# Optimization experiments

Measured on AMD Instinct MI355X. Metric: run time of the kernel, lower is better.

The kernel has to match this reference:

```python
import jax, jax.numpy as jnp
import numpy as np


def setup_inputs() -> dict:
    key = jax.random.key(0)
    k1, k2 = jax.random.split(key)
    x = jax.random.normal(k1, (16, 64, 224, 224), dtype=jnp.float32)
    # conv weight [out=1, in=2, kh=7, kw=7]; init roughly mimics small-normal init
    conv_w = jax.random.normal(k2, (1, 2, 7, 7), dtype=jnp.float32) * 0.01
    conv_b = jnp.zeros((1,), dtype=jnp.float32)
    return {"x": x, "conv_w": conv_w, "conv_b": conv_b}


def reference(x, conv_w, conv_b):
    # channel-wise mean and max -> [B, 2, H, W]
    avg_out = jnp.mean(x, axis=1, keepdims=True)
    max_out = jnp.max(x, axis=1, keepdims=True)
    feat = jnp.concatenate([avg_out, max_out], axis=1)
    # 2->1 channel 7x7 conv, padding 3 (same)
    y = jax.lax.conv_general_dilated(
        feat, conv_w,
        window_strides=(1, 1),
        padding=((3, 3), (3, 3)),
        dimension_numbers=("NCHW", "OIHW", "NCHW"),
    ) + conv_b[None, :, None, None]
    # sigmoid gate broadcast-multiplied back onto x
    return jax.nn.sigmoid(y) * x
```

## Files before the change

kernel.cpp:

```cpp
#include <hip/hip_runtime.h>
#include <math.h>

#define BB 16
#define CC 64
#define HH 224
#define WW 224
#define HWSZ (HH * WW)
#define HW4 (HWSZ / 4)
#define R 14
#define TILES (HH / R)
#define FR (R + 6)
#define FW 240
#define W4 (WW / 4)
#define T 512

__global__ __launch_bounds__(T) void fused_kernel(const float* __restrict__ x,
                                                  const float* __restrict__ cw,
                                                  const float* __restrict__ cb,
                                                  float* __restrict__ out) {
    __shared__ float fa[FR * FW];
    __shared__ float fm[FR * FW];
    __shared__ alignas(16) float gate[R * WW];
    __shared__ float wt[98];

    const int blk = blockIdx.x;
    const int b   = blk >> 4;
    const int tb  = blk & 15;
    const int h0  = tb * R;
    const int t   = threadIdx.x;

    for (int i = t; i < FR * FW; i += T) { fa[i] = 0.f; fm[i] = 0.f; }
    if (t < 98) wt[t] = cw[t];
    __syncthreads();

    const float4* xb = reinterpret_cast<const float4*>(x) + (size_t)b * (CC * HW4);
    for (int p = t; p < FR * W4; p += T) {
        int pr = p / W4;
        int pc = p - pr * W4;
        int gh = h0 - 3 + pr;
        if ((unsigned)gh >= (unsigned)HH) continue;
        const float4* xp = xb + gh * W4 + pc;
        float4 s = make_float4(0.f, 0.f, 0.f, 0.f);
        float4 m = make_float4(-INFINITY, -INFINITY, -INFINITY, -INFINITY);
#pragma unroll 8
        for (int c = 0; c < CC; ++c) {
            float4 u = xp[(size_t)c * HW4];
            s.x += u.x; s.y += u.y; s.z += u.z; s.w += u.w;
            m.x = fmaxf(m.x, u.x); m.y = fmaxf(m.y, u.y);
            m.z = fmaxf(m.z, u.z); m.w = fmaxf(m.w, u.w);
        }
        const float inv = 1.0f / 64.0f;
        int o = pr * FW + 3 + pc * 4;
        fa[o + 0] = s.x * inv; fa[o + 1] = s.y * inv;
        fa[o + 2] = s.z * inv; fa[o + 3] = s.w * inv;
        fm[o + 0] = m.x; fm[o + 1] = m.y; fm[o + 2] = m.z; fm[o + 3] = m.w;
    }
    __syncthreads();

    const float bias = cb[0];
    for (int p = t; p < R * WW; p += T) {
        int r = p / WW;
        int w = p - r * WW;
        float acc = bias;
#pragma unroll
        for (int kh = 0; kh < 7; ++kh) {
            int ro = (r + kh) * FW + w;
#pragma unroll
            for (int kw = 0; kw < 7; ++kw) {
                acc = fmaf(fa[ro + kw], wt[kh * 7 + kw], acc);
                acc = fmaf(fm[ro + kw], wt[49 + kh * 7 + kw], acc);
            }
        }
        gate[p] = 1.0f / (1.0f + expf(-acc));
    }
    __syncthreads();

    float4* ob = reinterpret_cast<float4*>(out) + (size_t)b * (CC * HW4);
    const float4* g4 = reinterpret_cast<const float4*>(gate);
    const int NP = R * W4;
    for (int i = t; i < CC * NP; i += T) {
        int c  = i / NP;
        int p  = i - c * NP;
        int pr = p / W4;
        int pc = p - pr * W4;
        size_t off = (size_t)c * HW4 + (size_t)(h0 + pr) * W4 + pc;
        float4 v = xb[off];
        float4 g = g4[p];
        v.x *= g.x; v.y *= g.y; v.z *= g.z; v.w *= g.w;
        ob[off] = v;
    }
}

extern "C" void kernel_launch(void* const* d_in, const int* in_sizes, int n_in,
                              void* d_out, int out_size, void* d_ws, size_t ws_size,
                              hipStream_t stream) {
    const float* x  = (const float*)d_in[0];
    const float* cw = (const float*)d_in[1];
    const float* cb = (const float*)d_in[2];
    float* out = (float*)d_out;

    fused_kernel<<<BB * TILES, T, 0, stream>>>(x, cw, cb, out);
}
```

Baseline: 410.7 us.

## Halve row tile, remap blocks across XCDs, and use nontemporal output stores

Halves the rows per block from 14 to 7, doubling the grid to 512 blocks, and sets a min-blocks-per-SM launch bound so more blocks run at once and the GPU fills better. Block indices are permuted so consecutive launch IDs are spread across the 8 XCD groups, and the output is written with nontemporal stores so it does not pollute cache. The trade-off is that the 3-row conv halo now makes up a larger share of each tile, so more input is re-read during the channel reduction (13 rows loaded per 7 output rows instead of 20 per 14).

```diff
diff --git a/kernel.cpp b/kernel.cpp
--- a/kernel.cpp
+++ b/kernel.cpp
@@ -7,53 +7,57 @@
 #define WW 224
 #define HWSZ (HH * WW)
 #define HW4 (HWSZ / 4)
-#define R 14
+#define R 7
 #define TILES (HH / R)
 #define FR (R + 6)
 #define FW 240
 #define W4 (WW / 4)
 #define T 512
+#define NBLK (BB * TILES)
 
-__global__ __launch_bounds__(T) void fused_kernel(const float* __restrict__ x,
-                                                  const float* __restrict__ cw,
-                                                  const float* __restrict__ cb,
-                                                  float* __restrict__ out) {
+typedef float f32x4 __attribute__((ext_vector_type(4)));
+
+__global__ __launch_bounds__(T, 4) void fused_kernel(const float* __restrict__ x,
+                                                     const float* __restrict__ cw,
+                                                     const float* __restrict__ cb,
+                                                     float* __restrict__ out) {
     __shared__ float fa[FR * FW];
     __shared__ float fm[FR * FW];
     __shared__ alignas(16) float gate[R * WW];
     __shared__ float wt[98];
 
-    const int blk = blockIdx.x;
-    const int b   = blk >> 4;
-    const int tb  = blk & 15;
-    const int h0  = tb * R;
-    const int t   = threadIdx.x;
+    const int blk0 = blockIdx.x;
+    const int blk  = (blk0 & 7) * (NBLK / 8) + (blk0 >> 3);
+    const int b    = blk >> 5;
+    const int tb   = blk & 31;
+    const int h0   = tb * R;
+    const int t    = threadIdx.x;
 
     for (int i = t; i < FR * FW; i += T) { fa[i] = 0.f; fm[i] = 0.f; }
     if (t < 98) wt[t] = cw[t];
     __syncthreads();
 
-    const float4* xb = reinterpret_cast<const float4*>(x) + (size_t)b * (CC * HW4);
+    const f32x4* xb = reinterpret_cast<const f32x4*>(x) + (size_t)b * (CC * HW4);
     for (int p = t; p < FR * W4; p += T) {
         int pr = p / W4;
         int pc = p - pr * W4;
         int gh = h0 - 3 + pr;
         if ((unsigned)gh >= (unsigned)HH) continue;
-        const float4* xp = xb + gh * W4 + pc;
-        float4 s = make_float4(0.f, 0.f, 0.f, 0.f);
-        float4 m = make_float4(-INFINITY, -INFINITY, -INFINITY, -INFINITY);
+        const f32x4* xp = xb + gh * W4 + pc;
+        f32x4 s = {0.f, 0.f, 0.f, 0.f};
+        f32x4 m = {-INFINITY, -INFINITY, -INFINITY, -INFINITY};
 #pragma unroll 8
         for (int c = 0; c < CC; ++c) {
-            float4 u = xp[(size_t)c * HW4];
-            s.x += u.x; s.y += u.y; s.z += u.z; s.w += u.w;
-            m.x = fmaxf(m.x, u.x); m.y = fmaxf(m.y, u.y);
-            m.z = fmaxf(m.z, u.z); m.w = fmaxf(m.w, u.w);
+            f32x4 u = xp[(size_t)c * HW4];
+            s += u;
+            m[0] = fmaxf(m[0], u[0]); m[1] = fmaxf(m[1], u[1]);
+            m[2] = fmaxf(m[2], u[2]); m[3] = fmaxf(m[3], u[3]);
         }
         const float inv = 1.0f / 64.0f;
         int o = pr * FW + 3 + pc * 4;
-        fa[o + 0] = s.x * inv; fa[o + 1] = s.y * inv;
-        fa[o + 2] = s.z * inv; fa[o + 3] = s.w * inv;
-        fm[o + 0] = m.x; fm[o + 1] = m.y; fm[o + 2] = m.z; fm[o + 3] = m.w;
+        fa[o + 0] = s[0] * inv; fa[o + 1] = s[1] * inv;
+        fa[o + 2] = s[2] * inv; fa[o + 3] = s[3] * inv;
+        fm[o + 0] = m[0]; fm[o + 1] = m[1]; fm[o + 2] = m[2]; fm[o + 3] = m[3];
     }
     __syncthreads();
 
@@ -75,8 +79,8 @@
     }
     __syncthreads();
 
-    float4* ob = reinterpret_cast<float4*>(out) + (size_t)b * (CC * HW4);
-    const float4* g4 = reinterpret_cast<const float4*>(gate);
+    f32x4* ob = reinterpret_cast<f32x4*>(out) + (size_t)b * (CC * HW4);
+    const f32x4* g4 = reinterpret_cast<const f32x4*>(gate);
     const int NP = R * W4;
     for (int i = t; i < CC * NP; i += T) {
         int c  = i / NP;
@@ -84,10 +88,10 @@
         int pr = p / W4;
         int pc = p - pr * W4;
         size_t off = (size_t)c * HW4 + (size_t)(h0 + pr) * W4 + pc;
-        float4 v = xb[off];
-        float4 g = g4[p];
-        v.x *= g.x; v.y *= g.y; v.z *= g.z; v.w *= g.w;
-        ob[off] = v;
+        f32x4 v = xb[off];
+        f32x4 g = g4[p];
+        v *= g;
+        __builtin_nontemporal_store(v, ob + off);
     }
 }
 
@@ -99,5 +103,5 @@
     const float* cb = (const float*)d_in[2];
     float* out = (float*)d_out;
 
-    fused_kernel<<<BB * TILES, T, 0, stream>>>(x, cw, cb, out);
+    fused_kernel<<<NBLK, T, 0, stream>>>(x, cw, cb, out);
 }
```

New measurement: 378.2 us. 1.09x faster.
